# Optimization experiments

Hardware: AMD Instinct MI355X
Metric: run time of the kernel (lower is better)

## Reference

```python
import jax, jax.numpy as jnp
import numpy as np

D_MODEL = 1024
NUM_HEADS = 16
D_HEAD = D_MODEL // NUM_HEADS  # 64
LAMBDA_INIT = 0.8
EPS = 1e-5


def setup_inputs() -> dict:
    key = jax.random.key(0)
    ks = jax.random.split(key, 10)
    B, N = 2, 2048
    # Xavier-uniform-ish scale for the projection weights
    def xav(k, shape):
        fan_in, fan_out = shape[0], shape[1]
        lim = np.sqrt(6.0 / (fan_in + fan_out))
        return jax.random.uniform(k, shape, jnp.float32, -lim, lim)
    return {
        "X": jax.random.normal(ks[0], (B, N, D_MODEL), jnp.float32),
        "Wq": xav(ks[1], (D_MODEL, 2 * D_MODEL)),
        "Wk": xav(ks[2], (D_MODEL, 2 * D_MODEL)),
        "Wv": xav(ks[3], (D_MODEL, 2 * D_MODEL)),
        "Wo": xav(ks[4], (2 * D_MODEL, D_MODEL)),
        "lambda_q1": jax.random.normal(ks[5], (NUM_HEADS, D_HEAD), jnp.float32),
        "lambda_k1": jax.random.normal(ks[6], (NUM_HEADS, D_HEAD), jnp.float32),
        "lambda_q2": jax.random.normal(ks[7], (NUM_HEADS, D_HEAD), jnp.float32),
        "lambda_k2": jax.random.normal(ks[8], (NUM_HEADS, D_HEAD), jnp.float32),
        "rms_scale": jnp.ones((2 * D_HEAD,), jnp.float32),
    }


def reference(X, Wq, Wk, Wv, Wo, lambda_q1, lambda_k1, lambda_q2, lambda_k2, rms_scale):
    B, N, _ = X.shape
    H, Dh = NUM_HEADS, D_HEAD
    # projections -> [B, H, N, 2*Dh]
    Q = (X @ Wq).reshape(B, N, H, 2 * Dh).transpose(0, 2, 1, 3)
    K = (X @ Wk).reshape(B, N, H, 2 * Dh).transpose(0, 2, 1, 3)
    V = (X @ Wv).reshape(B, N, H, 2 * Dh).transpose(0, 2, 1, 3)
    Q1, Q2 = Q[..., :Dh], Q[..., Dh:]
    K1, K2 = K[..., :Dh], K[..., Dh:]
    # learned lambda per head
    lam = (jnp.exp(jnp.sum(lambda_q1 * lambda_k1, -1))
           - jnp.exp(jnp.sum(lambda_q2 * lambda_k2, -1))
           + LAMBDA_INIT)  # [H]
    scaling = 1.0 / np.sqrt(Dh)
    causal = jnp.tril(jnp.ones((N, N), bool))  # [N, N]
    neg_inf = jnp.float32(-jnp.inf)
    A1 = jnp.einsum('bhqd,bhkd->bhqk', Q1, K1) * scaling
    A2 = jnp.einsum('bhqd,bhkd->bhqk', Q2, K2) * scaling
    A1 = jnp.where(causal, A1, neg_inf)
    A2 = jnp.where(causal, A2, neg_inf)
    attn = jax.nn.softmax(A1, axis=-1) - lam[None, :, None, None] * jax.nn.softmax(A2, axis=-1)
    O = jnp.einsum('bhqk,bhkd->bhqd', attn, V)  # [B, H, N, 2*Dh]
    # per-(batch,head,pos) RMSNorm over the 2*Dh channel dim
    rms = jnp.sqrt(jnp.mean(O * O, axis=-1, keepdims=True) + EPS)
    O = O / rms * rms_scale
    O = O * (1.0 - LAMBDA_INIT)
    O = O.transpose(0, 2, 1, 3).reshape(B, N, H * 2 * Dh)
    return O @ Wo
```

## Files before the change

### kernel.cpp

```cpp
#include <hip/hip_runtime.h>
#include <hip/hip_bf16.h>

#define DM   1024
#define NH   16
#define DH   64
#define NSEQ 2048
#define NBATCH 2
#define ROWS (NBATCH*NSEQ)
#define QKVN (2*DM)
#define STR3 (3*DM*2)

typedef __attribute__((ext_vector_type(8))) short short8;
typedef __attribute__((ext_vector_type(4))) float f32x4;
typedef __attribute__((ext_vector_type(4))) unsigned short u16x4;

__device__ __forceinline__ unsigned short f2bf(float x) {
  union { float f; unsigned u; } v; v.f = x;
  unsigned r = v.u + 0x7FFFu + ((v.u >> 16) & 1u);
  return (unsigned short)(r >> 16);
}

__device__ __forceinline__ float exp2a(float x) {
  float r; asm("v_exp_f32 %0, %1" : "=v"(r) : "v"(x)); return r;
}
__device__ __forceinline__ unsigned cvtpk(float lo, float hi) {
  unsigned d; asm("v_cvt_pk_bf16_f32 %0, %1, %2" : "=v"(d) : "v"(lo), "v"(hi)); return d;
}

__device__ __forceinline__ f32x4 mfma16(short8 a, short8 b, f32x4 c) {
  return __builtin_amdgcn_mfma_f32_16x16x32_bf16(a, b, c, 0, 0, 0);
}

#define GLL(src, dst) \
  __builtin_amdgcn_global_load_lds((const __attribute__((address_space(1))) void*)(src), \
                                   (__attribute__((address_space(3))) void*)(dst), 16, 0, 0)

#define WAITV(n) asm volatile("s_waitcnt vmcnt(" #n ")" ::: "memory")

__global__ void prep_fused(const float* __restrict__ X,
                           const float* __restrict__ Wq, const float* __restrict__ Wk,
                           const float* __restrict__ Wv, const float* __restrict__ Wo,
                           unsigned short* __restrict__ Xb,
                           unsigned short* __restrict__ Wt,
                           unsigned short* __restrict__ Wot) {
  const int z = blockIdx.z;
  const int tx = threadIdx.x, ty = threadIdx.y;

  if (z == 4) {
    const int bid = blockIdx.y * 64 + blockIdx.x;
    const int t = ty * 32 + tx;
    #pragma unroll
    for (int j = 0; j < 2; ++j) {
      const int i = bid * 512 + j * 256 + t;
      f32x4 v = *(const f32x4*)(X + (size_t)i * 4);
      u16x4 o;
      #pragma unroll
      for (int k = 0; k < 4; ++k) o[k] = f2bf(v[k]);
      *(u16x4*)(Xb + (size_t)i * 4) = o;
    }
    return;
  }

  const float* in;
  unsigned short* out;
  int R, C, bx, by;
  if (z < 3) {
    in = (z == 0) ? Wq : (z == 1) ? Wk : Wv;
    out = Wt + (size_t)z * 2048 * 1024;
    R = DM; C = QKVN;
    bx = blockIdx.x; by = blockIdx.y;
  } else {
    in = Wo; out = Wot;
    R = QKVN; C = DM;
    bx = blockIdx.y; by = blockIdx.x;
  }

  __shared__ float tile[32][33];
  #pragma unroll
  for (int i = 0; i < 4; ++i)
    tile[ty + i*8][tx] = in[(size_t)(by*32 + ty + i*8) * C + bx*32 + tx];
  __syncthreads();
  #pragma unroll
  for (int i = 0; i < 4; ++i)
    out[(size_t)(bx*32 + ty + i*8) * R + by*32 + tx] = f2bf(tile[tx][ty + i*8]);
}

__global__ void transpose_v(const unsigned short* __restrict__ Vb, unsigned short* __restrict__ Vt) {
  __shared__ unsigned short tile[32][33];
  const int bx = blockIdx.x, by = blockIdx.y;
  const int tx = threadIdx.x, ty = threadIdx.y;
  #pragma unroll
  for (int i = 0; i < 4; ++i)
    tile[ty + i*8][tx] = Vb[(size_t)(by*32 + ty + i*8) * STR3 + bx*32 + tx];
  __syncthreads();
  #pragma unroll
  for (int i = 0; i < 4; ++i) {
    int colg = bx*32 + ty + i*8;
    int rowg = by*32 + tx;
    int hh = colg >> 7, dd = colg & 127;
    int bb = rowg >> 11, nn = rowg & 2047;
    Vt[(size_t)((bb*NH + hh)*128 + dd) * NSEQ + nn] = tile[tx][ty + i*8];
  }
}

__global__ void lam_kernel(const float* __restrict__ lq1, const float* __restrict__ lk1,
                           const float* __restrict__ lq2, const float* __restrict__ lk2,
                           float* __restrict__ lam) {
  int h = threadIdx.x >> 6, lane = threadIdx.x & 63;
  float p1 = lq1[h*64 + lane] * lk1[h*64 + lane];
  float p2 = lq2[h*64 + lane] * lk2[h*64 + lane];
  #pragma unroll
  for (int mk = 32; mk >= 1; mk >>= 1) {
    p1 += __shfl_xor(p1, mk);
    p2 += __shfl_xor(p2, mk);
  }
  if (lane == 0) lam[h] = expf(p1) - expf(p2) + 0.8f;
}

template <typename OT>
__global__ __launch_bounds__(512) void gemm8p(const unsigned short* __restrict__ A,
                                              const unsigned short* __restrict__ Bt,
                                              OT* __restrict__ C, int M, int N, int K, int ldc) {
  __shared__ __align__(16) unsigned short As[2][2][256*32];
  __shared__ __align__(16) unsigned short Bs[2][2][256*32];
  (void)M; (void)N;
  const int tid = threadIdx.x;
  const int wv = tid >> 6, lane = tid & 63;
  const int l15 = lane & 15, lg = lane >> 4;
  const int wm = wv >> 2, wn = wv & 3;

  const unsigned gx = gridDim.x;
  unsigned bid = blockIdx.y * gx + blockIdx.x;
  const unsigned cpx = (gx * gridDim.y) >> 3;
  bid = (bid & 7u) * cpx + (bid >> 3);
  const int m0 = (int)(bid / gx) * 256, n0 = (int)(bid % gx) * 256;

  const int NT = K >> 6;

  int rowS[2], subS[2];
  #pragma unroll
  for (int j = 0; j < 2; ++j) {
    const int c = j*512 + tid;
    rowS[j] = c >> 2;
    const int s = c & 3;
    subS[j] = (s ^ (rowS[j] & 3) ^ ((rowS[j] >> 2) & 3)) & 3;
  }
  const unsigned short* Ab = A  + (size_t)m0 * K;
  const unsigned short* Bb = Bt + (size_t)n0 * K;

  auto stA = [&](int b, int ks, int tt) {
    #pragma unroll
    for (int j = 0; j < 2; ++j)
      GLL(Ab + (size_t)rowS[j]*K + tt*64 + ks*32 + subS[j]*8,
          &As[b][ks][(j*512 + (wv << 6)) * 8]);
  };
  auto stB = [&](int b, int ks, int tt) {
    #pragma unroll
    for (int j = 0; j < 2; ++j)
      GLL(Bb + (size_t)rowS[j]*K + tt*64 + ks*32 + subS[j]*8,
          &Bs[b][ks][(j*512 + (wv << 6)) * 8]);
  };

  const int phys = ((lg ^ (l15 & 3) ^ ((l15 >> 2) & 3)) & 3) * 8;

  auto rdA = [&](int b, int ks, int Mh, short8* af) {
    #pragma unroll
    for (int m = 0; m < 4; ++m) {
      const int row = wm*128 + Mh*64 + m*16 + l15;
      af[m] = *(const short8*)(&As[b][ks][row*32 + phys]);
    }
  };
  auto rdB = [&](int b, int ks, short8* bf) {
    #pragma unroll
    for (int n = 0; n < 4; ++n) {
      const int row = wn*64 + n*16 + l15;
      bf[n] = *(const short8*)(&Bs[b][ks][row*32 + phys]);
    }
  };

  f32x4 acc[8][4];
  #pragma unroll
  for (int i = 0; i < 8; ++i)
    #pragma unroll
    for (int j = 0; j < 4; ++j) acc[i][j] = f32x4{0.f, 0.f, 0.f, 0.f};

  stA(0, 0, 0); stB(0, 0, 0); stA(0, 1, 0); stB(0, 1, 0);
  stA(1, 0, 1); stB(1, 0, 1);
  WAITV(4);
  __builtin_amdgcn_s_barrier();

  short8 af[4], bf[4];

#define MFMA_CLUSTER(MH)                                               \
    asm volatile("s_waitcnt lgkmcnt(0)" ::: "memory");                 \
    __builtin_amdgcn_sched_barrier(0);                                 \
    __builtin_amdgcn_s_setprio(1);                                     \
    _Pragma("unroll")                                                  \
    for (int m = 0; m < 4; ++m)                                        \
      _Pragma("unroll")                                                \
      for (int n = 0; n < 4; ++n)                                      \
        acc[(MH)*4+m][n] = mfma16(af[m], bf[n], acc[(MH)*4+m][n]);     \
    __builtin_amdgcn_s_setprio(0);                                     \
    __builtin_amdgcn_s_barrier();

  for (int t = 0; t < NT; t += 2) {
    const bool s2 = (t + 2 < NT);
    const bool s3 = (t + 3 < NT);

    rdA(0, 0, 0, af); rdB(0, 0, bf);
    stA(1, 1, t + 1);
    __builtin_amdgcn_s_barrier();
    MFMA_CLUSTER(0)
    rdA(0, 0, 1, af);
    stB(1, 1, t + 1);
    __builtin_amdgcn_s_barrier();
    MFMA_CLUSTER(1)
    rdA(0, 1, 0, af); rdB(0, 1, bf);
    if (s2) stA(0, 0, t + 2);
    __builtin_amdgcn_s_barrier();
    MFMA_CLUSTER(0)
    rdA(0, 1, 1, af);
    if (s2) { stB(0, 0, t + 2); WAITV(4); } else { WAITV(0); }
    __builtin_amdgcn_s_barrier();
    MFMA_CLUSTER(1)
    rdA(1, 0, 0, af); rdB(1, 0, bf);
    if (s2) stA(0, 1, t + 2);
    __builtin_amdgcn_s_barrier();
    MFMA_CLUSTER(0)
    rdA(1, 0, 1, af);
    if (s2) stB(0, 1, t + 2);
    __builtin_amdgcn_s_barrier();
    MFMA_CLUSTER(1)
    rdA(1, 1, 0, af); rdB(1, 1, bf);
    if (s3) stA(1, 0, t + 3);
    __builtin_amdgcn_s_barrier();
    MFMA_CLUSTER(0)
    rdA(1, 1, 1, af);
    if (s3) stB(1, 0, t + 3);
    WAITV(4);
    __builtin_amdgcn_s_barrier();
    MFMA_CLUSTER(1)
  }
#undef MFMA_CLUSTER

  #pragma unroll
  for (int mi = 0; mi < 8; ++mi)
    #pragma unroll
    for (int n = 0; n < 4; ++n)
      #pragma unroll
      for (int r = 0; r < 4; ++r) {
        const int row = m0 + wm*128 + (mi >> 2)*64 + (mi & 3)*16 + lg*4 + r;
        const int col = n0 + wn*64 + n*16 + l15;
        if constexpr (sizeof(OT) == 2)
          C[(size_t)row * ldc + col] = f2bf(acc[mi][n][r]);
        else
          C[(size_t)row * ldc + col] = acc[mi][n][r];
      }
}

template <typename OT>
__global__ __launch_bounds__(256) void gemm_bt(const unsigned short* __restrict__ A,
                                               const unsigned short* __restrict__ Bt,
                                               OT* __restrict__ C, int M, int N, int K) {
  __shared__ __align__(16) unsigned short As[128*32];
  __shared__ __align__(16) unsigned short Bs[128*32];
  const int tid = threadIdx.x;
  const int w = tid >> 6, lane = tid & 63;
  const int l15 = lane & 15, lg = lane >> 4;
  const int wr = w >> 1, wc = w & 1;

  const unsigned gx = gridDim.x;
  unsigned bid = blockIdx.y * gx + blockIdx.x;
  const unsigned cpx = (gx * gridDim.y) >> 3;
  bid = (bid & 7u) * cpx + (bid >> 3);
  const int m0 = (int)(bid / gx) * 128, n0 = (int)(bid % gx) * 128;

  f32x4 acc[4][4];
  #pragma unroll
  for (int i = 0; i < 4; ++i)
    #pragma unroll
    for (int j = 0; j < 4; ++j) acc[i][j] = f32x4{0.f, 0.f, 0.f, 0.f};

  for (int kt = 0; kt < K; kt += 32) {
    #pragma unroll
    for (int j = 0; j < 2; ++j) {
      int cbase = (j*4 + w) * 64;
      int c = cbase + lane;
      const unsigned short* ga = A + (size_t)(m0 + (c >> 2)) * K + kt + (c & 3) * 8;
      GLL(ga, As + cbase*8);
      const unsigned short* gb = Bt + (size_t)(n0 + (c >> 2)) * K + kt + (c & 3) * 8;
      GLL(gb, Bs + cbase*8);
    }
    __syncthreads();
    short8 af[4], bfr[4];
    #pragma unroll
    for (int m = 0; m < 4; ++m)
      af[m] = *(const short8*)(As + (wr*64 + m*16 + l15) * 32 + lg*8);
    #pragma unroll
    for (int n = 0; n < 4; ++n)
      bfr[n] = *(const short8*)(Bs + (wc*64 + n*16 + l15) * 32 + lg*8);
    #pragma unroll
    for (int m = 0; m < 4; ++m)
      #pragma unroll
      for (int n = 0; n < 4; ++n)
        acc[m][n] = mfma16(af[m], bfr[n], acc[m][n]);
    __syncthreads();
  }

  #pragma unroll
  for (int m = 0; m < 4; ++m)
    #pragma unroll
    for (int n = 0; n < 4; ++n)
      #pragma unroll
      for (int r = 0; r < 4; ++r) {
        int row = m0 + wr*64 + m*16 + lg*4 + r;
        int col = n0 + wc*64 + n*16 + l15;
        if constexpr (sizeof(OT) == 2)
          C[(size_t)row * N + col] = f2bf(acc[m][n][r]);
        else
          C[(size_t)row * N + col] = acc[m][n][r];
      }
}

__global__ __launch_bounds__(256) void diff_attn(const unsigned short* __restrict__ QKV,
                                                 const unsigned short* __restrict__ Vt,
                                                 const float* __restrict__ lam_arr,
                                                 const float* __restrict__ rms_scale,
                                                 unsigned short* __restrict__ O) {
  __shared__ __align__(16) unsigned short Ks[2][64*128];
  __shared__ __align__(16) unsigned short Vs[2][128*64];
  __shared__ __align__(16) unsigned short Plds[4][2][16*64];

  const unsigned bid = blockIdx.x;
  const int xcd = (int)(bid & 7u), idx = (int)(bid >> 3);
  const int bh = xcd * 4 + (idx >> 4);
  const int jj = idx & 15;

  const int b = bh >> 4, h = bh & 15;
  const int w = threadIdx.x >> 6, lane = threadIdx.x & 63;
  const int l15 = lane & 15, lg = lane >> 4;
  const float lam = lam_arr[h];

  const unsigned short* Qb  = QKV + (size_t)(b * NSEQ) * STR3 + h * 128;
  const unsigned short* Kb  = QKV + (size_t)(b * NSEQ) * STR3 + 2048 + h * 128;
  const unsigned short* Vtb = Vt + (size_t)bh * 128 * NSEQ;

  auto stage = [&](int bufi, int key0) {
    #pragma unroll
    for (int j = 0; j < 4; ++j) {
      const int t = j*4 + w;
      {
        const int row = t*4 + (lane >> 4);
        const int ck  = lane & 15;
        const int cks = (ck & 8) | ((ck ^ row) & 7);
        GLL(Kb + (size_t)(key0 + row) * STR3 + cks*8, &Ks[bufi][t*512]);
      }
      {
        const int row = t*8 + (lane >> 3);
        const int ck  = lane & 7;
        const int cks = (ck ^ row) & 7;
        GLL(Vtb + (size_t)row * NSEQ + key0 + cks*8, &Vs[bufi][t*512]);
      }
    }
  };

  char* pb0 = (char*)&Plds[w][0][0];
  char* pb1 = (char*)&Plds[w][1][0];
  const unsigned swz = (unsigned)((l15 & 7) << 4);
  const float qsc = 0.125f * 1.44269504088896340736f;
  const int kx0 = ((lg ^ l15) & 7) * 8;
  const int kx1 = (((4 + lg) ^ l15) & 7) * 8;

  for (int pass = 0; pass < 2; ++pass) {
    const int qt = pass ? jj : 31 - jj;
    const int q0 = qt * 64 + w * 16;

    short8 a1[2], a2[2];
    #pragma unroll
    for (int kc = 0; kc < 2; ++kc) {
      const unsigned short* qp = Qb + (size_t)(q0 + l15) * STR3 + kc*32 + lg*8;
      short8 r1 = *(const short8*)qp;
      short8 r2 = *(const short8*)(qp + 64);
      #pragma unroll
      for (int j = 0; j < 8; j += 2) {
        union { unsigned u; float f; } x0, x1, y0, y1;
        x0.u = ((unsigned)(unsigned short)r1[j]) << 16;
        x1.u = ((unsigned)(unsigned short)r1[j+1]) << 16;
        y0.u = ((unsigned)(unsigned short)r2[j]) << 16;
        y1.u = ((unsigned)(unsigned short)r2[j+1]) << 16;
        unsigned d1 = cvtpk(x0.f * qsc, x1.f * qsc);
        unsigned d2 = cvtpk(y0.f * qsc, y1.f * qsc);
        a1[kc][j]   = (short)(unsigned short)(d1 & 0xffffu);
        a1[kc][j+1] = (short)(unsigned short)(d1 >> 16);
        a2[kc][j]   = (short)(unsigned short)(d2 & 0xffffu);
        a2[kc][j+1] = (short)(unsigned short)(d2 >> 16);
      }
    }

    f32x4 o1[8], o2[8];
    #pragma unroll
    for (int i = 0; i < 8; ++i) { o1[i] = f32x4{0,0,0,0}; o2[i] = f32x4{0,0,0,0}; }
    float m1 = -3e38f, l1 = 0.f, m2 = -3e38f, l2 = 0.f;

    stage(0, 0);
    __syncthreads();
    int buf = 0;

    for (int kb = 0; kb <= qt; ++kb) {
      const int key0 = kb * 64;
      if (kb < qt) stage(buf ^ 1, key0 + 64);

      f32x4 st1[4], st2[4];
      #pragma unroll
      for (int nb = 0; nb < 4; ++nb) { st1[nb] = f32x4{0,0,0,0}; st2[nb] = f32x4{0,0,0,0}; }
      __builtin_amdgcn_s_setprio(1);
      #pragma unroll
      for (int nb = 0; nb < 4; ++nb) {
        const unsigned short* krow = &Ks[buf][nb*2048 + l15*128];
        short8 k10 = *(const short8*)(krow + kx0);
        short8 k11 = *(const short8*)(krow + kx1);
        short8 k20 = *(const short8*)(krow + kx0 + 64);
        short8 k21 = *(const short8*)(krow + kx1 + 64);
        st1[nb] = mfma16(k10, a1[0], st1[nb]);
        st1[nb] = mfma16(k11, a1[1], st1[nb]);
        st2[nb] = mfma16(k20, a2[0], st2[nb]);
        st2[nb] = mfma16(k21, a2[1], st2[nb]);
      }
      __builtin_amdgcn_s_setprio(0);

      if (kb == qt) {
        #pragma unroll
        for (int nb = 0; nb < 4; ++nb)
          #pragma unroll
          for (int r = 0; r < 4; ++r)
            if (key0 + nb*16 + lg*4 + r > q0 + l15) { st1[nb][r] = -3e38f; st2[nb][r] = -3e38f; }
      }

      float tm1 = -3e38f, tm2 = -3e38f;
      #pragma unroll
      for (int nb = 0; nb < 4; ++nb)
        #pragma unroll
        for (int r = 0; r < 4; ++r) {
          tm1 = fmaxf(tm1, st1[nb][r]); tm2 = fmaxf(tm2, st2[nb][r]);
        }
      tm1 = fmaxf(tm1, __shfl_xor(tm1, 16));
      tm1 = fmaxf(tm1, __shfl_xor(tm1, 32));
      tm2 = fmaxf(tm2, __shfl_xor(tm2, 16));
      tm2 = fmaxf(tm2, __shfl_xor(tm2, 32));

      if (__any(tm1 > m1 + 8.f)) {
        const float nm = fmaxf(m1, tm1);
        const float e = exp2a(m1 - nm);
        m1 = nm; l1 *= e;
        float er[4];
        #pragma unroll
        for (int r = 0; r < 4; ++r) er[r] = __shfl(e, lg*4 + r);
        #pragma unroll
        for (int i = 0; i < 8; ++i)
          #pragma unroll
          for (int r = 0; r < 4; ++r) o1[i][r] *= er[r];
      }
      if (__any(tm2 > m2 + 8.f)) {
        const float nm = fmaxf(m2, tm2);
        const float e = exp2a(m2 - nm);
        m2 = nm; l2 *= e;
        float er[4];
        #pragma unroll
        for (int r = 0; r < 4; ++r) er[r] = __shfl(e, lg*4 + r);
        #pragma unroll
        for (int i = 0; i < 8; ++i)
          #pragma unroll
          for (int r = 0; r < 4; ++r) o2[i][r] *= er[r];
      }

      float ts1 = 0.f, ts2 = 0.f;
      #pragma unroll
      for (int nb = 0; nb < 4; ++nb)
        #pragma unroll
        for (int r = 0; r < 4; ++r) {
          st1[nb][r] = exp2a(st1[nb][r] - m1); ts1 += st1[nb][r];
          st2[nb][r] = exp2a(st2[nb][r] - m2); ts2 += st2[nb][r];
        }
      ts1 += __shfl_xor(ts1, 16); ts1 += __shfl_xor(ts1, 32); l1 += ts1;
      ts2 += __shfl_xor(ts2, 16); ts2 += __shfl_xor(ts2, 32); l2 += ts2;

      #pragma unroll
      for (int nb = 0; nb < 4; ++nb) {
        const unsigned off = (unsigned)(l15*128 + nb*32 + lg*8) ^ swz;
        *(uint2*)(pb0 + off) = make_uint2(cvtpk(st1[nb][0], st1[nb][1]),
                                          cvtpk(st1[nb][2], st1[nb][3]));
        *(uint2*)(pb1 + off) = make_uint2(cvtpk(st2[nb][0], st2[nb][1]),
                                          cvtpk(st2[nb][2], st2[nb][3]));
      }
      asm volatile("s_waitcnt lgkmcnt(0)" ::: "memory");
      __builtin_amdgcn_sched_barrier(0);
      short8 pa1[2], pa2[2];
      #pragma unroll
      for (int kc = 0; kc < 2; ++kc) {
        const unsigned off = (unsigned)(l15*128 + kc*64 + lg*16) ^ swz;
        pa1[kc] = *(const short8*)(pb0 + off);
        pa2[kc] = *(const short8*)(pb1 + off);
      }
      __builtin_amdgcn_sched_barrier(0);

      __builtin_amdgcn_s_setprio(1);
      #pragma unroll
      for (int i = 0; i < 8; ++i) {
        const unsigned short* vrow = &Vs[buf][(i*16 + l15) * 64];
        const short8 b0 = *(const short8*)(vrow + kx0);
        const short8 b1 = *(const short8*)(vrow + kx1);
        o1[i] = mfma16(pa1[0], b0, o1[i]);
        o2[i] = mfma16(pa2[0], b0, o2[i]);
        o1[i] = mfma16(pa1[1], b1, o1[i]);
        o2[i] = mfma16(pa2[1], b1, o2[i]);
      }
      __builtin_amdgcn_s_setprio(0);

      __syncthreads();
      buf ^= 1;
    }

    float i1r[4], i2r[4];
    {
      const float inv1 = 1.f / l1, inv2 = 1.f / l2;
      #pragma unroll
      for (int r = 0; r < 4; ++r) {
        i1r[r] = __shfl(inv1, lg*4 + r);
        i2r[r] = __shfl(inv2, lg*4 + r);
      }
    }
    float ov[8][4];
    float ssq[4] = {0.f, 0.f, 0.f, 0.f};
    #pragma unroll
    for (int i = 0; i < 8; ++i)
      #pragma unroll
      for (int r = 0; r < 4; ++r) {
        float v = o1[i][r] * i1r[r] - lam * (o2[i][r] * i2r[r]);
        ov[i][r] = v;
        ssq[r] += v * v;
      }
    #pragma unroll
    for (int r = 0; r < 4; ++r)
      #pragma unroll
      for (int mk = 1; mk < 16; mk <<= 1) ssq[r] += __shfl_xor(ssq[r], mk);
    float rr[4];
    #pragma unroll
    for (int r = 0; r < 4; ++r) rr[r] = rsqrtf(ssq[r] * (1.f/128.f) + 1e-5f) * 0.2f;
    #pragma unroll
    for (int i = 0; i < 8; ++i) {
      const float sc = rms_scale[i*16 + l15];
      #pragma unroll
      for (int r = 0; r < 4; ++r) {
        const int q = q0 + lg*4 + r;
        O[(size_t)(b*NSEQ + q) * QKVN + h*128 + i*16 + l15] = f2bf(ov[i][r] * rr[r] * sc);
      }
    }
  }
}

extern "C" void kernel_launch(void* const* d_in, const int* in_sizes, int n_in,
                              void* d_out, int out_size, void* d_ws, size_t ws_size,
                              hipStream_t stream) {
  (void)in_sizes; (void)n_in; (void)out_size; (void)ws_size;
  const float* X   = (const float*)d_in[0];
  const float* Wq  = (const float*)d_in[1];
  const float* Wk  = (const float*)d_in[2];
  const float* Wv  = (const float*)d_in[3];
  const float* Wo  = (const float*)d_in[4];
  const float* lq1 = (const float*)d_in[5];
  const float* lk1 = (const float*)d_in[6];
  const float* lq2 = (const float*)d_in[7];
  const float* lk2 = (const float*)d_in[8];
  const float* rs  = (const float*)d_in[9];
  float* out = (float*)d_out;

  char* ws = (char*)d_ws;
  const size_t MB = 1ull << 20;
  unsigned short* Xb  = (unsigned short*)(ws);
  unsigned short* Wt  = (unsigned short*)(ws + 8*MB);
  unsigned short* Wot = (unsigned short*)(ws + 20*MB);
  unsigned short* QKV = (unsigned short*)(ws + 24*MB);
  unsigned short* Ob  = (unsigned short*)(ws + 72*MB);
  float*          lamp = (float*)(ws + 88*MB);
  unsigned short* Vt  = (unsigned short*)(ws);

  prep_fused<<<dim3(64, 32, 5), dim3(32, 8), 0, stream>>>(X, Wq, Wk, Wv, Wo, Xb, Wt, Wot);
  lam_kernel<<<1, 1024, 0, stream>>>(lq1, lk1, lq2, lk2, lamp);

  gemm8p<unsigned short><<<dim3(STR3/256, ROWS/256), 512, 0, stream>>>(
      Xb, Wt, QKV, ROWS, STR3, DM, STR3);

  transpose_v<<<dim3(QKVN/32, ROWS/32), dim3(32,8), 0, stream>>>(QKV + 4096, Vt);

  diff_attn<<<dim3(512), 256, 0, stream>>>(QKV, Vt, lamp, rs, Ob);

  gemm_bt<float><<<dim3(DM/128, ROWS/128), 256, 0, stream>>>(Ob, Wot, out, ROWS, DM, QKVN);
}
```

Measured before the change: 236.7 us.

## Interleave the two softmax branches in diff-attention and fold lambda into prep

```diff
diff --git a/kernel.cpp b/kernel.cpp
--- a/kernel.cpp
+++ b/kernel.cpp
@@ -40,9 +40,12 @@
 __global__ void prep_fused(const float* __restrict__ X,
                            const float* __restrict__ Wq, const float* __restrict__ Wk,
                            const float* __restrict__ Wv, const float* __restrict__ Wo,
+                           const float* __restrict__ lq1, const float* __restrict__ lk1,
+                           const float* __restrict__ lq2, const float* __restrict__ lk2,
                            unsigned short* __restrict__ Xb,
                            unsigned short* __restrict__ Wt,
-                           unsigned short* __restrict__ Wot) {
+                           unsigned short* __restrict__ Wot,
+                           float* __restrict__ lamp) {
   const int z = blockIdx.z;
   const int tx = threadIdx.x, ty = threadIdx.y;
 
@@ -57,6 +60,18 @@
       #pragma unroll
       for (int k = 0; k < 4; ++k) o[k] = f2bf(v[k]);
       *(u16x4*)(Xb + (size_t)i * 4) = o;
+    }
+    if (bid < 4) {
+      const int wv = t >> 6, lane = t & 63;
+      const int h = bid * 4 + wv;
+      float p1 = lq1[h*64 + lane] * lk1[h*64 + lane];
+      float p2 = lq2[h*64 + lane] * lk2[h*64 + lane];
+      #pragma unroll
+      for (int mk = 32; mk >= 1; mk >>= 1) {
+        p1 += __shfl_xor(p1, mk);
+        p2 += __shfl_xor(p2, mk);
+      }
+      if (lane == 0) lamp[h] = expf(p1) - expf(p2) + 0.8f;
     }
     return;
   }
@@ -103,20 +118,6 @@
   }
 }
 
-__global__ void lam_kernel(const float* __restrict__ lq1, const float* __restrict__ lk1,
-                           const float* __restrict__ lq2, const float* __restrict__ lk2,
-                           float* __restrict__ lam) {
-  int h = threadIdx.x >> 6, lane = threadIdx.x & 63;
-  float p1 = lq1[h*64 + lane] * lk1[h*64 + lane];
-  float p2 = lq2[h*64 + lane] * lk2[h*64 + lane];
-  #pragma unroll
-  for (int mk = 32; mk >= 1; mk >>= 1) {
-    p1 += __shfl_xor(p1, mk);
-    p2 += __shfl_xor(p2, mk);
-  }
-  if (lane == 0) lam[h] = expf(p1) - expf(p2) + 0.8f;
-}
-
 template <typename OT>
 __global__ __launch_bounds__(512) void gemm8p(const unsigned short* __restrict__ A,
                                               const unsigned short* __restrict__ Bt,
@@ -410,21 +411,17 @@
       const int key0 = kb * 64;
       if (kb < qt) stage(buf ^ 1, key0 + 64);
 
-      f32x4 st1[4], st2[4];
-      #pragma unroll
-      for (int nb = 0; nb < 4; ++nb) { st1[nb] = f32x4{0,0,0,0}; st2[nb] = f32x4{0,0,0,0}; }
+      const unsigned short* Kbase = &Ks[buf][l15*128];
+
+      f32x4 st1[4];
+      #pragma unroll
+      for (int nb = 0; nb < 4; ++nb) st1[nb] = f32x4{0,0,0,0};
       __builtin_amdgcn_s_setprio(1);
       #pragma unroll
       for (int nb = 0; nb < 4; ++nb) {
-        const unsigned short* krow = &Ks[buf][nb*2048 + l15*128];
-        short8 k10 = *(const short8*)(krow + kx0);
-        short8 k11 = *(const short8*)(krow + kx1);
-        short8 k20 = *(const short8*)(krow + kx0 + 64);
-        short8 k21 = *(const short8*)(krow + kx1 + 64);
-        st1[nb] = mfma16(k10, a1[0], st1[nb]);
-        st1[nb] = mfma16(k11, a1[1], st1[nb]);
-        st2[nb] = mfma16(k20, a2[0], st2[nb]);
-        st2[nb] = mfma16(k21, a2[1], st2[nb]);
+        const unsigned short* krow = Kbase + nb*2048;
+        st1[nb] = mfma16(*(const short8*)(krow + kx0), a1[0], st1[nb]);
+        st1[nb] = mfma16(*(const short8*)(krow + kx1), a1[1], st1[nb]);
       }
       __builtin_amdgcn_s_setprio(0);
 
@@ -433,20 +430,32 @@
         for (int nb = 0; nb < 4; ++nb)
           #pragma unroll
           for (int r = 0; r < 4; ++r)
-            if (key0 + nb*16 + lg*4 + r > q0 + l15) { st1[nb][r] = -3e38f; st2[nb][r] = -3e38f; }
-      }
-
-      float tm1 = -3e38f, tm2 = -3e38f;
-      #pragma unroll
-      for (int nb = 0; nb < 4; ++nb)
+            if (key0 + nb*16 + lg*4 + r > q0 + l15) st1[nb][r] = -3e38f;
+      }
+
+      f32x4 st2[4];
+      #pragma unroll
+      for (int nb = 0; nb < 4; ++nb) st2[nb] = f32x4{0,0,0,0};
+      float tm1;
+      {
+        f32x4 mA, mB;
         #pragma unroll
         for (int r = 0; r < 4; ++r) {
-          tm1 = fmaxf(tm1, st1[nb][r]); tm2 = fmaxf(tm2, st2[nb][r]);
+          mA[r] = fmaxf(st1[0][r], st1[1][r]);
+          mB[r] = fmaxf(st1[2][r], st1[3][r]);
         }
+        #pragma unroll
+        for (int r = 0; r < 4; ++r) mA[r] = fmaxf(mA[r], mB[r]);
+        tm1 = fmaxf(fmaxf(mA[0], mA[1]), fmaxf(mA[2], mA[3]));
+      }
+      #pragma unroll
+      for (int nb = 0; nb < 4; ++nb) {
+        const unsigned short* krow = Kbase + nb*2048;
+        st2[nb] = mfma16(*(const short8*)(krow + kx0 + 64), a2[0], st2[nb]);
+        st2[nb] = mfma16(*(const short8*)(krow + kx1 + 64), a2[1], st2[nb]);
+      }
       tm1 = fmaxf(tm1, __shfl_xor(tm1, 16));
       tm1 = fmaxf(tm1, __shfl_xor(tm1, 32));
-      tm2 = fmaxf(tm2, __shfl_xor(tm2, 16));
-      tm2 = fmaxf(tm2, __shfl_xor(tm2, 32));
 
       if (__any(tm1 > m1 + 8.f)) {
         const float nm = fmaxf(m1, tm1);
@@ -460,6 +469,63 @@
           #pragma unroll
           for (int r = 0; r < 4; ++r) o1[i][r] *= er[r];
       }
+
+      #pragma unroll
+      for (int nb = 0; nb < 4; ++nb)
+        #pragma unroll
+        for (int r = 0; r < 4; ++r) st1[nb][r] = exp2a(st1[nb][r] - m1);
+      {
+        f32x4 s4 = (st1[0] + st1[1]) + (st1[2] + st1[3]);
+        float ts1 = (s4[0] + s4[1]) + (s4[2] + s4[3]);
+        ts1 += __shfl_xor(ts1, 16); ts1 += __shfl_xor(ts1, 32); l1 += ts1;
+      }
+      #pragma unroll
+      for (int nb = 0; nb < 4; ++nb) {
+        const unsigned off = (unsigned)(l15*128 + nb*32 + lg*8) ^ swz;
+        *(uint2*)(pb0 + off) = make_uint2(cvtpk(st1[nb][0], st1[nb][1]),
+                                          cvtpk(st1[nb][2], st1[nb][3]));
+      }
+
+      if (kb == qt) {
+        #pragma unroll
+        for (int nb = 0; nb < 4; ++nb)
+          #pragma unroll
+          for (int r = 0; r < 4; ++r)
+            if (key0 + nb*16 + lg*4 + r > q0 + l15) st2[nb][r] = -3e38f;
+      }
+
+      asm volatile("s_waitcnt lgkmcnt(0)" ::: "memory");
+      __builtin_amdgcn_sched_barrier(0);
+      short8 pa1[2];
+      pa1[0] = *(const short8*)(pb0 + ((unsigned)(l15*128 + 0*64 + lg*16) ^ swz));
+      pa1[1] = *(const short8*)(pb0 + ((unsigned)(l15*128 + 1*64 + lg*16) ^ swz));
+      __builtin_amdgcn_sched_barrier(0);
+
+      short8 bva0[8], bva1[8];
+      #pragma unroll
+      for (int i = 0; i < 8; ++i) {
+        const unsigned short* vrow = &Vs[buf][(i*16 + l15) * 64];
+        bva0[i] = *(const short8*)(vrow + kx0);
+        bva1[i] = *(const short8*)(vrow + kx1);
+        o1[i] = mfma16(pa1[0], bva0[i], o1[i]);
+        o1[i] = mfma16(pa1[1], bva1[i], o1[i]);
+      }
+
+      float tm2;
+      {
+        f32x4 mA, mB;
+        #pragma unroll
+        for (int r = 0; r < 4; ++r) {
+          mA[r] = fmaxf(st2[0][r], st2[1][r]);
+          mB[r] = fmaxf(st2[2][r], st2[3][r]);
+        }
+        #pragma unroll
+        for (int r = 0; r < 4; ++r) mA[r] = fmaxf(mA[r], mB[r]);
+        tm2 = fmaxf(fmaxf(mA[0], mA[1]), fmaxf(mA[2], mA[3]));
+      }
+      tm2 = fmaxf(tm2, __shfl_xor(tm2, 16));
+      tm2 = fmaxf(tm2, __shfl_xor(tm2, 32));
+
       if (__any(tm2 > m2 + 8.f)) {
         const float nm = fmaxf(m2, tm2);
         const float e = exp2a(m2 - nm);
@@ -473,46 +539,34 @@
           for (int r = 0; r < 4; ++r) o2[i][r] *= er[r];
       }
 
-      float ts1 = 0.f, ts2 = 0.f;
       #pragma unroll
       for (int nb = 0; nb < 4; ++nb)
         #pragma unroll
-        for (int r = 0; r < 4; ++r) {
-          st1[nb][r] = exp2a(st1[nb][r] - m1); ts1 += st1[nb][r];
-          st2[nb][r] = exp2a(st2[nb][r] - m2); ts2 += st2[nb][r];
-        }
-      ts1 += __shfl_xor(ts1, 16); ts1 += __shfl_xor(ts1, 32); l1 += ts1;
-      ts2 += __shfl_xor(ts2, 16); ts2 += __shfl_xor(ts2, 32); l2 += ts2;
-
+        for (int r = 0; r < 4; ++r) st2[nb][r] = exp2a(st2[nb][r] - m2);
+      {
+        f32x4 s4 = (st2[0] + st2[1]) + (st2[2] + st2[3]);
+        float ts2 = (s4[0] + s4[1]) + (s4[2] + s4[3]);
+        ts2 += __shfl_xor(ts2, 16); ts2 += __shfl_xor(ts2, 32); l2 += ts2;
+      }
       #pragma unroll
       for (int nb = 0; nb < 4; ++nb) {
         const unsigned off = (unsigned)(l15*128 + nb*32 + lg*8) ^ swz;
-        *(uint2*)(pb0 + off) = make_uint2(cvtpk(st1[nb][0], st1[nb][1]),
-                                          cvtpk(st1[nb][2], st1[nb][3]));
         *(uint2*)(pb1 + off) = make_uint2(cvtpk(st2[nb][0], st2[nb][1]),
                                           cvtpk(st2[nb][2], st2[nb][3]));
       }
+
       asm volatile("s_waitcnt lgkmcnt(0)" ::: "memory");
       __builtin_amdgcn_sched_barrier(0);
-      short8 pa1[2], pa2[2];
-      #pragma unroll
-      for (int kc = 0; kc < 2; ++kc) {
-        const unsigned off = (unsigned)(l15*128 + kc*64 + lg*16) ^ swz;
-        pa1[kc] = *(const short8*)(pb0 + off);
-        pa2[kc] = *(const short8*)(pb1 + off);
-      }
+      short8 pa2[2];
+      pa2[0] = *(const short8*)(pb1 + ((unsigned)(l15*128 + 0*64 + lg*16) ^ swz));
+      pa2[1] = *(const short8*)(pb1 + ((unsigned)(l15*128 + 1*64 + lg*16) ^ swz));
       __builtin_amdgcn_sched_barrier(0);
 
       __builtin_amdgcn_s_setprio(1);
       #pragma unroll
       for (int i = 0; i < 8; ++i) {
-        const unsigned short* vrow = &Vs[buf][(i*16 + l15) * 64];
-        const short8 b0 = *(const short8*)(vrow + kx0);
-        const short8 b1 = *(const short8*)(vrow + kx1);
-        o1[i] = mfma16(pa1[0], b0, o1[i]);
-        o2[i] = mfma16(pa2[0], b0, o2[i]);
-        o1[i] = mfma16(pa1[1], b1, o1[i]);
-        o2[i] = mfma16(pa2[1], b1, o2[i]);
+        o2[i] = mfma16(pa2[0], bva0[i], o2[i]);
+        o2[i] = mfma16(pa2[1], bva1[i], o2[i]);
       }
       __builtin_amdgcn_s_setprio(0);
 
@@ -584,8 +638,8 @@
   float*          lamp = (float*)(ws + 88*MB);
   unsigned short* Vt  = (unsigned short*)(ws);
 
-  prep_fused<<<dim3(64, 32, 5), dim3(32, 8), 0, stream>>>(X, Wq, Wk, Wv, Wo, Xb, Wt, Wot);
-  lam_kernel<<<1, 1024, 0, stream>>>(lq1, lk1, lq2, lk2, lamp);
+  prep_fused<<<dim3(64, 32, 5), dim3(32, 8), 0, stream>>>(
+      X, Wq, Wk, Wv, Wo, lq1, lk1, lq2, lk2, Xb, Wt, Wot, lamp);
 
   gemm8p<unsigned short><<<dim3(STR3/256, ROWS/256), 512, 0, stream>>>(
       Xb, Wt, QKV, ROWS, STR3, DM, STR3);
```

Measured after the change: 289.0 us. 22.1% more time.
